# Performance work log

Measured on AMD Instinct MI355X. Metric: run time of the kernel, lower is better.

## Reference

```python
import jax, jax.numpy as jnp
import numpy as np

DIM = 2048
DIM_VISUAL = 1024
HEADS = 16
DIM_HEAD = 64
INNER = HEADS * DIM_HEAD  # 1024
EPS = 1e-5


def setup_inputs() -> dict:
    key = jax.random.key(0)
    ks = jax.random.split(key, 6)
    y = jax.random.normal(ks[0], (4, 2048, DIM), dtype=jnp.float32)
    visual_features = jax.random.normal(ks[1], (4, 8, 64, DIM_VISUAL), dtype=jnp.float32)
    ln_g = jnp.ones((DIM,), dtype=jnp.float32)
    ln_b = jnp.zeros((DIM,), dtype=jnp.float32)
    Wq = jax.random.normal(ks[2], (DIM, INNER), dtype=jnp.float32) * 0.02
    Wkv = jax.random.normal(ks[3], (DIM_VISUAL, 2 * INNER), dtype=jnp.float32) * 0.02
    Wo = jax.random.normal(ks[4], (INNER, DIM), dtype=jnp.float32) * 0.02
    return {"y": y, "visual_features": visual_features, "ln_g": ln_g, "ln_b": ln_b,
            "Wq": Wq, "Wkv": Wkv, "Wo": Wo}


def reference(y, visual_features, ln_g, ln_b, Wq, Wkv, Wo):
    scale = DIM_HEAD ** (-0.5)
    b, t, nq, dv = visual_features.shape
    # LayerNorm over last dim
    mu = jnp.mean(y, axis=-1, keepdims=True)
    var = jnp.mean(jnp.square(y - mu), axis=-1, keepdims=True)
    yn = (y - mu) * jax.lax.rsqrt(var + EPS) * ln_g + ln_b
    q = (yn @ Wq) * scale                      # (b, n, inner)
    vis = visual_features.reshape(b, t * nq, dv)
    kv = vis @ Wkv                             # (b, m, 2*inner)
    k, v = jnp.split(kv, 2, axis=-1)
    # split heads: b n (h d) -> b h n d
    split = lambda x: x.reshape(x.shape[0], x.shape[1], HEADS, DIM_HEAD).transpose(0, 2, 1, 3)
    q, k, v = split(q), split(k), split(v)
    sim = jnp.einsum('bhid,bhjd->bhij', q, k)
    alphas = jax.nn.softmax(sim, axis=-1)      # amax-subtract softmax (stable)
    out = jnp.einsum('bhij,bhjd->bhid', alphas, v)
    out = out.transpose(0, 2, 1, 3).reshape(out.shape[0], out.shape[2], INNER)
    return out @ Wo
```

## Files before the change

kernel.cpp:

```cpp
#include <hip/hip_runtime.h>
#include <stdint.h>

typedef unsigned short u16;
typedef __bf16 bfrag __attribute__((ext_vector_type(8)));
typedef float f32x4 __attribute__((ext_vector_type(4)));
typedef u16 u16x4 __attribute__((ext_vector_type(4)));

__device__ __forceinline__ float bf2f(u16 u) {
  union { unsigned i; float f; } x; x.i = ((unsigned)u) << 16; return x.f;
}
__device__ __forceinline__ u16 f2bf(float f) {
  union { unsigned i; float f; } x; x.f = f;
  unsigned r = x.i + 0x7fffu + ((x.i >> 16) & 1u);
  return (u16)(r >> 16);
}
__device__ __forceinline__ unsigned packbf(float lo, float hi) {
  return (unsigned)f2bf(lo) | ((unsigned)f2bf(hi) << 16);
}

__device__ __forceinline__ f32x4 mfma16(bfrag a, bfrag b, f32x4 c) {
  return __builtin_amdgcn_mfma_f32_16x16x32_bf16(a, b, c, 0, 0, 0);
}

__device__ __forceinline__ void gl_lds16(const u16* g, const u16* l) {
  __builtin_amdgcn_global_load_lds(
      (const __attribute__((address_space(1))) unsigned int*)g,
      (__attribute__((address_space(3))) unsigned int*)l, 16, 0, 0);
}

__device__ __forceinline__ void xcd_swizzle(int& bx, int& by) {
  int gx = gridDim.x, nwg = gx * gridDim.y;
  int flat = by * gx + bx;
  int cpx = nwg >> 3;
  int swz = (flat & 7) * cpx + (flat >> 3);
  bx = swz % gx;
  by = swz / gx;
}

__global__ __launch_bounds__(256) void k_transpose(const float* __restrict__ in,
                                                   u16* __restrict__ out, int R, int C) {
  __shared__ u16 tile[32][33];
  int c0 = blockIdx.x * 32, r0 = blockIdx.y * 32;
  int tx = threadIdx.x, ty = threadIdx.y;
#pragma unroll
  for (int i = 0; i < 4; ++i)
    tile[ty + i * 8][tx] = f2bf(in[(size_t)(r0 + ty + i * 8) * C + c0 + tx]);
  __syncthreads();
#pragma unroll
  for (int i = 0; i < 4; ++i)
    out[(size_t)(c0 + ty + i * 8) * R + r0 + tx] = tile[tx][ty + i * 8];
}

__global__ __launch_bounds__(256) void k_cast(const float* __restrict__ in,
                                              u16* __restrict__ out, int n8) {
  int i = blockIdx.x * 256 + threadIdx.x;
  if (i >= n8) return;
  float4 a = *(const float4*)(in + (size_t)i * 8);
  float4 b = *(const float4*)(in + (size_t)i * 8 + 4);
  uint4 ov; u16* po = (u16*)&ov;
  po[0] = f2bf(a.x); po[1] = f2bf(a.y); po[2] = f2bf(a.z); po[3] = f2bf(a.w);
  po[4] = f2bf(b.x); po[5] = f2bf(b.y); po[6] = f2bf(b.z); po[7] = f2bf(b.w);
  *(uint4*)(out + (size_t)i * 8) = ov;
}

__global__ __launch_bounds__(256) void k_layernorm(const float* __restrict__ y,
                                                   const float* __restrict__ g,
                                                   const float* __restrict__ bb,
                                                   u16* __restrict__ yn) {
  int row = blockIdx.x, t = threadIdx.x;
  const float* yr = y + (size_t)row * 2048 + t * 8;
  float4 v0 = *(const float4*)(yr);
  float4 v1 = *(const float4*)(yr + 4);
  float x[8] = {v0.x, v0.y, v0.z, v0.w, v1.x, v1.y, v1.z, v1.w};
  float s = 0.f, ss = 0.f;
#pragma unroll
  for (int j = 0; j < 8; ++j) { s += x[j]; ss += x[j] * x[j]; }
#pragma unroll
  for (int off = 32; off > 0; off >>= 1) {
    s += __shfl_down(s, off);
    ss += __shfl_down(ss, off);
  }
  __shared__ float rs[4], rq[4];
  int lane = t & 63, wid = t >> 6;
  if (lane == 0) { rs[wid] = s; rq[wid] = ss; }
  __syncthreads();
  float S = rs[0] + rs[1] + rs[2] + rs[3];
  float Q = rq[0] + rq[1] + rq[2] + rq[3];
  float mean = S * (1.f / 2048.f);
  float var = Q * (1.f / 2048.f) - mean * mean;
  float rstd = rsqrtf(var + 1e-5f);
  float4 g0 = *(const float4*)(g + t * 8);
  float4 g1 = *(const float4*)(g + t * 8 + 4);
  float4 b0 = *(const float4*)(bb + t * 8);
  float4 b1 = *(const float4*)(bb + t * 8 + 4);
  float gg[8] = {g0.x, g0.y, g0.z, g0.w, g1.x, g1.y, g1.z, g1.w};
  float bv[8] = {b0.x, b0.y, b0.z, b0.w, b1.x, b1.y, b1.z, b1.w};
  uint4 ov; u16* po = (u16*)&ov;
#pragma unroll
  for (int j = 0; j < 8; ++j)
    po[j] = f2bf((x[j] - mean) * rstd * gg[j] + bv[j]);
  *(uint4*)(yn + (size_t)row * 2048 + t * 8) = ov;
}

template <bool F32OUT>
__global__ __launch_bounds__(256) void k_gemm_bt(const u16* __restrict__ A,
                                                 const u16* __restrict__ Bt,
                                                 void* __restrict__ Cv,
                                                 int M, int N, int K, float scale) {
  __shared__ __align__(16) u16 As[2][128 * 64];
  __shared__ __align__(16) u16 Bs[2][128 * 64];
  int t = threadIdx.x, lane = t & 63, wid = t >> 6;
  int wm = wid >> 1, wn = wid & 1;
  int bx = blockIdx.x, by = blockIdx.y;
  xcd_swizzle(bx, by);
  int m0 = by * 128, n0 = bx * 128;
  int lr = lane & 15, lg = lane >> 4;
  int sk = lr & 7;

  f32x4 acc[4][4];
#pragma unroll
  for (int i = 0; i < 4; ++i)
#pragma unroll
    for (int j = 0; j < 4; ++j) acc[i][j] = (f32x4){0.f, 0.f, 0.f, 0.f};

  int srow[4], scol[4], sbase[4];
#pragma unroll
  for (int j = 0; j < 4; ++j) {
    int s0 = (wid * 4 + j) * 64;
    int s = s0 + lane;
    srow[j] = s >> 3;
    scol[j] = ((s & 7) ^ (srow[j] & 7)) * 8;
    sbase[j] = s0 * 8;
  }

#pragma unroll
  for (int j = 0; j < 4; ++j) {
    gl_lds16(A + (size_t)(m0 + srow[j]) * K + scol[j], As[0] + sbase[j]);
    gl_lds16(Bt + (size_t)(n0 + srow[j]) * K + scol[j], Bs[0] + sbase[j]);
  }
  __syncthreads();

  int nk = K >> 6;
  for (int kt = 0; kt < nk; ++kt) {
    int cur = kt & 1;
    if (kt + 1 < nk) {
      int k0 = (kt + 1) << 6;
#pragma unroll
      for (int j = 0; j < 4; ++j) {
        gl_lds16(A + (size_t)(m0 + srow[j]) * K + k0 + scol[j], As[cur ^ 1] + sbase[j]);
        gl_lds16(Bt + (size_t)(n0 + srow[j]) * K + k0 + scol[j], Bs[cur ^ 1] + sbase[j]);
      }
    }
    const u16* as = As[cur];
    const u16* bs = Bs[cur];
#pragma unroll
    for (int kk = 0; kk < 2; ++kk) {
      bfrag a[4], b[4];
#pragma unroll
      for (int i = 0; i < 4; ++i)
        a[i] = *(const bfrag*)(as + (wm * 64 + i * 16 + lr) * 64 + (((kk * 4 + lg) ^ sk) * 8));
#pragma unroll
      for (int j = 0; j < 4; ++j)
        b[j] = *(const bfrag*)(bs + (wn * 64 + j * 16 + lr) * 64 + (((kk * 4 + lg) ^ sk) * 8));
#pragma unroll
      for (int i = 0; i < 4; ++i)
#pragma unroll
        for (int j = 0; j < 4; ++j)
          acc[i][j] = mfma16(a[i], b[j], acc[i][j]);
    }
    if (kt + 1 < nk) __syncthreads();
  }
#pragma unroll
  for (int i = 0; i < 4; ++i)
#pragma unroll
    for (int j = 0; j < 4; ++j) {
      int r0 = m0 + wm * 64 + i * 16 + lg * 4;
      int c0 = n0 + wn * 64 + j * 16 + lr;
#pragma unroll
      for (int r = 0; r < 4; ++r) {
        float v = scale * acc[i][j][r];
        if (F32OUT)
          ((float*)Cv)[(size_t)(r0 + r) * N + c0] = v;
        else
          ((u16*)Cv)[(size_t)(r0 + r) * N + c0] = f2bf(v);
      }
    }
}

__global__ __launch_bounds__(256) void k_gemm_kv(const u16* __restrict__ A,
                                                 const u16* __restrict__ Bt,
                                                 u16* __restrict__ Kb,
                                                 u16* __restrict__ Vtb) {
  const int K = 1024;
  __shared__ __align__(16) u16 As[2][128 * 64];
  __shared__ __align__(16) u16 Bs[2][128 * 64];
  int t = threadIdx.x, lane = t & 63, wid = t >> 6;
  int wm = wid >> 1, wn = wid & 1;
  int bx = blockIdx.x, by = blockIdx.y;
  xcd_swizzle(bx, by);
  int m0 = by * 128, n0 = bx * 128;
  int lr = lane & 15, lg = lane >> 4;
  int sk = lr & 7;

  f32x4 acc[4][4];
#pragma unroll
  for (int i = 0; i < 4; ++i)
#pragma unroll
    for (int j = 0; j < 4; ++j) acc[i][j] = (f32x4){0.f, 0.f, 0.f, 0.f};

  int srow[4], scol[4], sbase[4];
#pragma unroll
  for (int j = 0; j < 4; ++j) {
    int s0 = (wid * 4 + j) * 64;
    int s = s0 + lane;
    srow[j] = s >> 3;
    scol[j] = ((s & 7) ^ (srow[j] & 7)) * 8;
    sbase[j] = s0 * 8;
  }

#pragma unroll
  for (int j = 0; j < 4; ++j) {
    gl_lds16(A + (size_t)(m0 + srow[j]) * K + scol[j], As[0] + sbase[j]);
    gl_lds16(Bt + (size_t)(n0 + srow[j]) * K + scol[j], Bs[0] + sbase[j]);
  }
  __syncthreads();

  int nk = K >> 6;
  for (int kt = 0; kt < nk; ++kt) {
    int cur = kt & 1;
    if (kt + 1 < nk) {
      int k0 = (kt + 1) << 6;
#pragma unroll
      for (int j = 0; j < 4; ++j) {
        gl_lds16(A + (size_t)(m0 + srow[j]) * K + k0 + scol[j], As[cur ^ 1] + sbase[j]);
        gl_lds16(Bt + (size_t)(n0 + srow[j]) * K + k0 + scol[j], Bs[cur ^ 1] + sbase[j]);
      }
    }
    const u16* as = As[cur];
    const u16* bs = Bs[cur];
#pragma unroll
    for (int kk = 0; kk < 2; ++kk) {
      bfrag a[4], b[4];
#pragma unroll
      for (int i = 0; i < 4; ++i)
        a[i] = *(const bfrag*)(as + (wm * 64 + i * 16 + lr) * 64 + (((kk * 4 + lg) ^ sk) * 8));
#pragma unroll
      for (int j = 0; j < 4; ++j)
        b[j] = *(const bfrag*)(bs + (wn * 64 + j * 16 + lr) * 64 + (((kk * 4 + lg) ^ sk) * 8));
#pragma unroll
      for (int i = 0; i < 4; ++i)
#pragma unroll
        for (int j = 0; j < 4; ++j)
          acc[i][j] = mfma16(a[i], b[j], acc[i][j]);
    }
    if (kt + 1 < nk) __syncthreads();
  }
#pragma unroll
  for (int i = 0; i < 4; ++i)
#pragma unroll
    for (int j = 0; j < 4; ++j) {
      int r0 = m0 + wm * 64 + i * 16 + lg * 4;
      int c0 = n0 + wn * 64 + j * 16 + lr;
      if (c0 < 1024) {
#pragma unroll
        for (int r = 0; r < 4; ++r)
          Kb[(size_t)(r0 + r) * 1024 + c0] = f2bf(acc[i][j][r]);
      } else {
        int d = c0 - 1024;
        int hh = d >> 6, dd = d & 63;
        int bq = r0 >> 9, kvp = r0 & 511;
        u16x4 pk;
#pragma unroll
        for (int r = 0; r < 4; ++r) pk[r] = f2bf(acc[i][j][r]);
        *(u16x4*)(Vtb + ((size_t)(bq * 16 + hh) * 64 + dd) * 512 + kvp) = pk;
      }
    }
}

__global__ __launch_bounds__(256, 2) void k_attn(const u16* __restrict__ q,
                                                 const u16* __restrict__ kb,
                                                 const u16* __restrict__ vt,
                                                 u16* __restrict__ ao) {
  __shared__ __align__(16) u16 Ks[2][128 * 64];
  __shared__ __align__(16) u16 Vt[2][64 * 128];
  int t = threadIdx.x, lane = t & 63, wid = t >> 6;
  int lr = lane & 15, lg = lane >> 4;
  int sk = lr & 7;
  int a_ = lg >> 1, b_ = lg & 1;
  int bh = blockIdx.y, b = bh >> 4, h = bh & 15;
  int q0 = blockIdx.x * 128 + wid * 32;

  const u16* qg = q + (size_t)(b * 2048 + q0) * 1024 + h * 64;
  bfrag qf[2][2];
#pragma unroll
  for (int rt = 0; rt < 2; ++rt)
#pragma unroll
    for (int kk = 0; kk < 2; ++kk)
      qf[rt][kk] = *(const bfrag*)(qg + (size_t)(rt * 16 + lr) * 1024 + kk * 32 + lg * 8);

  f32x4 o[2][4];
#pragma unroll
  for (int rt = 0; rt < 2; ++rt)
#pragma unroll
    for (int dt = 0; dt < 4; ++dt) o[rt][dt] = (f32x4){0.f, 0.f, 0.f, 0.f};
  float m_s[2] = {-1e30f, -1e30f}, l_s[2] = {0.f, 0.f};

  const u16* kgb = kb + (size_t)(b * 512) * 1024 + h * 64;
  const u16* vgb = vt + (size_t)bh * 64 * 512;

  int krow[4], kcol[4], kbase[4];
#pragma unroll
  for (int j = 0; j < 4; ++j) {
    int g = wid * 4 + j;
    int s = g * 64 + lane;
    krow[j] = s >> 3;
    kcol[j] = ((s & 7) ^ (krow[j] & 7)) * 8;
    kbase[j] = g * 512;
  }
  int vd = (threadIdx.x >> 4) & 3;

#pragma unroll
  for (int j = 0; j < 4; ++j)
    gl_lds16(kgb + (size_t)krow[j] * 1024 + kcol[j], Ks[0] + kbase[j]);
#pragma unroll
  for (int j = 0; j < 4; ++j) {
    int g = wid * 4 + j;
    int d = g * 4 + (lane >> 4);
    int p = lane & 15;
    gl_lds16(vgb + (size_t)d * 512 + ((p ^ (d & 7)) * 8), Vt[0] + g * 512);
  }
  __syncthreads();

  for (int it = 0; it < 4; ++it) {
    int cur = it & 1;
    if (it + 1 < 4) {
      int kv1 = (it + 1) * 128;
#pragma unroll
      for (int j = 0; j < 4; ++j)
        gl_lds16(kgb + (size_t)(kv1 + krow[j]) * 1024 + kcol[j], Ks[cur ^ 1] + kbase[j]);
#pragma unroll
      for (int j = 0; j < 4; ++j) {
        int g = wid * 4 + j;
        int d = g * 4 + (lane >> 4);
        int p = lane & 15;
        gl_lds16(vgb + (size_t)d * 512 + kv1 + ((p ^ (d & 7)) * 8), Vt[cur ^ 1] + g * 512);
      }
    }
    const u16* ks = Ks[cur];
    const u16* vtl = Vt[cur];

#pragma unroll
    for (int rt = 0; rt < 2; ++rt) {
      f32x4 s[8];
#pragma unroll
      for (int ct = 0; ct < 8; ++ct) {
        s[ct] = (f32x4){0.f, 0.f, 0.f, 0.f};
#pragma unroll
        for (int kk = 0; kk < 2; ++kk) {
          bfrag kf = *(const bfrag*)(ks + (ct * 16 + lr) * 64 + (((kk * 4 + lg) ^ sk) * 8));
          s[ct] = mfma16(kf, qf[rt][kk], s[ct]);
        }
      }
      float mloc = -1e30f;
#pragma unroll
      for (int ct = 0; ct < 8; ++ct)
#pragma unroll
        for (int r = 0; r < 4; ++r) mloc = fmaxf(mloc, s[ct][r]);
      mloc = fmaxf(mloc, __shfl_xor(mloc, 16));
      mloc = fmaxf(mloc, __shfl_xor(mloc, 32));
      float mn = fmaxf(m_s[rt], mloc);
      float scq = __expf(m_s[rt] - mn);
      float ps = 0.f;
#pragma unroll
      for (int ct = 0; ct < 8; ++ct)
#pragma unroll
        for (int r = 0; r < 4; ++r) {
          float p = __expf(s[ct][r] - mn);
          s[ct][r] = p;
          ps += p;
        }
      ps += __shfl_xor(ps, 16);
      ps += __shfl_xor(ps, 32);
      l_s[rt] = l_s[rt] * scq + ps;
      m_s[rt] = mn;
      float sc4[4];
#pragma unroll
      for (int r = 0; r < 4; ++r) sc4[r] = __shfl(scq, (lane & 48) | (lg * 4 + r));
#pragma unroll
      for (int dt = 0; dt < 4; ++dt)
#pragma unroll
        for (int r = 0; r < 4; ++r) o[rt][dt][r] *= sc4[r];

      unsigned w0[8], w1[8];
#pragma unroll
      for (int ct = 0; ct < 8; ++ct) {
        w0[ct] = packbf(s[ct][0], s[ct][1]);
        w1[ct] = packbf(s[ct][2], s[ct][3]);
      }
      bfrag pf[4];
#pragma unroll
      for (int kt = 0; kt < 4; ++kt) {
        unsigned c0w0 = w0[2 * kt], c0w1 = w1[2 * kt];
        unsigned c1w0 = w0[2 * kt + 1], c1w1 = w1[2 * kt + 1];
        unsigned s0 = a_ ? c0w0 : c1w0;
        unsigned s1 = a_ ? c0w1 : c1w1;
        unsigned k0 = a_ ? c1w0 : c0w0;
        unsigned k1 = a_ ? c1w1 : c0w1;
        unsigned r0 = (unsigned)__shfl_xor((int)s0, 32);
        unsigned r1 = (unsigned)__shfl_xor((int)s1, 32);
        unsigned x0 = (a_ == b_) ? r0 : k0;
        unsigned x1 = (a_ == b_) ? r1 : k1;
        unsigned kk0 = (a_ == b_) ? k0 : r0;
        unsigned kk1 = (a_ == b_) ? k1 : r1;
        unsigned q0_ = (unsigned)__shfl_xor((int)x0, 16);
        unsigned q1_ = (unsigned)__shfl_xor((int)x1, 16);
        union { unsigned u[4]; bfrag f; } uf;
        uf.u[0] = b_ ? q0_ : kk0;
        uf.u[1] = b_ ? q1_ : kk1;
        uf.u[2] = b_ ? kk0 : q0_;
        uf.u[3] = b_ ? kk1 : q1_;
        pf[kt] = uf.f;
      }
#pragma unroll
      for (int dt = 0; dt < 4; ++dt)
#pragma unroll
        for (int kt = 0; kt < 4; ++kt) {
          int d = dt * 16 + lr;
          bfrag vfb = *(const bfrag*)(vtl + d * 128 + (((kt * 4 + lg) ^ (d & 7)) * 8));
          o[rt][dt] = mfma16(pf[kt], vfb, o[rt][dt]);
        }
    }
    if (it + 1 < 4) __syncthreads();
  }

#pragma unroll
  for (int rt = 0; rt < 2; ++rt) {
    float invq = 1.f / l_s[rt];
    float i4[4];
#pragma unroll
    for (int r = 0; r < 4; ++r) i4[r] = __shfl(invq, (lane & 48) | (lg * 4 + r));
#pragma unroll
    for (int dt = 0; dt < 4; ++dt)
#pragma unroll
      for (int r = 0; r < 4; ++r)
        ao[(size_t)(b * 2048 + q0 + rt * 16 + lg * 4 + r) * 1024 + h * 64 + dt * 16 + lr] =
            f2bf(o[rt][dt][r] * i4[r]);
  }
}

extern "C" void kernel_launch(void* const* d_in, const int* in_sizes, int n_in,
                              void* d_out, int out_size, void* d_ws, size_t ws_size,
                              hipStream_t stream) {
  const float* y   = (const float*)d_in[0];
  const float* vf  = (const float*)d_in[1];
  const float* g   = (const float*)d_in[2];
  const float* bb  = (const float*)d_in[3];
  const float* Wq  = (const float*)d_in[4];
  const float* Wkv = (const float*)d_in[5];
  const float* Wo  = (const float*)d_in[6];
  float* out = (float*)d_out;
  char* ws = (char*)d_ws;

  u16* qb   = (u16*)(ws + 0ull);
  u16* kbuf = (u16*)(ws + 16777216ull);
  u16* vtb  = (u16*)(ws + 20971520ull);
  u16* aob  = (u16*)(ws + 25165824ull);
  u16* wqT  = (u16*)(ws + 41943040ull);
  u16* wkvT = (u16*)(ws + 46137344ull);
  u16* woT  = (u16*)(ws + 50331648ull);
  u16* vfb  = (u16*)(ws + 54525952ull);
  u16* yn = (u16*)d_out;

  dim3 tb(32, 8, 1);
  k_transpose<<<dim3(1024 / 32, 2048 / 32, 1), tb, 0, stream>>>(Wq, wqT, 2048, 1024);
  k_transpose<<<dim3(2048 / 32, 1024 / 32, 1), tb, 0, stream>>>(Wkv, wkvT, 1024, 2048);
  k_transpose<<<dim3(2048 / 32, 1024 / 32, 1), tb, 0, stream>>>(Wo, woT, 1024, 2048);
  k_cast<<<(2048 * 1024 / 8 + 255) / 256, 256, 0, stream>>>(vf, vfb, 2048 * 1024 / 8);
  k_layernorm<<<8192, 256, 0, stream>>>(y, g, bb, yn);
  k_gemm_bt<false><<<dim3(1024 / 128, 8192 / 128, 1), 256, 0, stream>>>(yn, wqT, qb, 8192, 1024, 2048, 0.125f);
  k_gemm_kv<<<dim3(2048 / 128, 2048 / 128, 1), 256, 0, stream>>>(vfb, wkvT, kbuf, vtb);
  k_attn<<<dim3(16, 64, 1), 256, 0, stream>>>(qb, kbuf, vtb, aob);
  k_gemm_bt<true><<<dim3(2048 / 128, 8192 / 128, 1), 256, 0, stream>>>(aob, woT, out, 8192, 2048, 1024, 1.0f);
}
```

Measured before the change: 178.1 us.

## Deepen GEMM prefetch pipeline and share K/V fragments across query tiles

```diff
diff --git a/kernel.cpp b/kernel.cpp
--- a/kernel.cpp
+++ b/kernel.cpp
@@ -102,74 +102,91 @@
   *(uint4*)(yn + (size_t)row * 2048 + t * 8) = ov;
 }
 
+__device__ __forceinline__ void gemm_pipe(const u16* __restrict__ A,
+                                          const u16* __restrict__ Bt,
+                                          int K, int m0, int n0,
+                                          int wm, int wn, int lr, int lg,
+                                          int wid, int lane,
+                                          f32x4 (&acc)[4][4]) {
+  __shared__ __align__(16) u16 As[2][128 * 64];
+  __shared__ __align__(16) u16 Bs[2][128 * 64];
+  int sk = lr & 7;
+  int srow[4], scol[4], sbase[4];
+#pragma unroll
+  for (int j = 0; j < 4; ++j) {
+    int s0 = (wid * 4 + j) * 64;
+    int s = s0 + lane;
+    srow[j] = s >> 3;
+    scol[j] = ((s & 7) ^ (srow[j] & 7)) * 8;
+    sbase[j] = s0 * 8;
+  }
+  int nk = K >> 6;
+#pragma unroll
+  for (int pt = 0; pt < 2; ++pt)
+#pragma unroll
+    for (int j = 0; j < 4; ++j) {
+      gl_lds16(A + (size_t)(m0 + srow[j]) * K + pt * 64 + scol[j], As[pt] + sbase[j]);
+      gl_lds16(Bt + (size_t)(n0 + srow[j]) * K + pt * 64 + scol[j], Bs[pt] + sbase[j]);
+    }
+  for (int tt = 0; tt < nk; ++tt) {
+    if (tt + 1 < nk)
+      asm volatile("s_waitcnt vmcnt(8)" ::: "memory");
+    else
+      asm volatile("s_waitcnt vmcnt(0)" ::: "memory");
+    __builtin_amdgcn_s_barrier();
+    __builtin_amdgcn_sched_barrier(0);
+    const u16* as = As[tt & 1];
+    const u16* bs = Bs[tt & 1];
+#pragma unroll
+    for (int kk = 0; kk < 2; ++kk) {
+      bfrag a[4], b[4];
+#pragma unroll
+      for (int i = 0; i < 4; ++i)
+        a[i] = *(const bfrag*)(as + (wm * 64 + i * 16 + lr) * 64 + (((kk * 4 + lg) ^ sk) * 8));
+#pragma unroll
+      for (int j = 0; j < 4; ++j)
+        b[j] = *(const bfrag*)(bs + (wn * 64 + j * 16 + lr) * 64 + (((kk * 4 + lg) ^ sk) * 8));
+      __builtin_amdgcn_s_setprio(1);
+#pragma unroll
+      for (int i = 0; i < 4; ++i)
+#pragma unroll
+        for (int j = 0; j < 4; ++j)
+          acc[i][j] = mfma16(a[i], b[j], acc[i][j]);
+      __builtin_amdgcn_s_setprio(0);
+    }
+    asm volatile("s_waitcnt lgkmcnt(0)" ::: "memory");
+    __builtin_amdgcn_s_barrier();
+    __builtin_amdgcn_sched_barrier(0);
+    if (tt + 2 < nk) {
+      int k0 = (tt + 2) * 64;
+#pragma unroll
+      for (int j = 0; j < 4; ++j) {
+        gl_lds16(A + (size_t)(m0 + srow[j]) * K + k0 + scol[j], As[tt & 1] + sbase[j]);
+        gl_lds16(Bt + (size_t)(n0 + srow[j]) * K + k0 + scol[j], Bs[tt & 1] + sbase[j]);
+      }
+    }
+  }
+}
+
 template <bool F32OUT>
 __global__ __launch_bounds__(256) void k_gemm_bt(const u16* __restrict__ A,
                                                  const u16* __restrict__ Bt,
                                                  void* __restrict__ Cv,
                                                  int M, int N, int K, float scale) {
-  __shared__ __align__(16) u16 As[2][128 * 64];
-  __shared__ __align__(16) u16 Bs[2][128 * 64];
   int t = threadIdx.x, lane = t & 63, wid = t >> 6;
   int wm = wid >> 1, wn = wid & 1;
   int bx = blockIdx.x, by = blockIdx.y;
   xcd_swizzle(bx, by);
   int m0 = by * 128, n0 = bx * 128;
   int lr = lane & 15, lg = lane >> 4;
-  int sk = lr & 7;
-
   f32x4 acc[4][4];
 #pragma unroll
   for (int i = 0; i < 4; ++i)
 #pragma unroll
     for (int j = 0; j < 4; ++j) acc[i][j] = (f32x4){0.f, 0.f, 0.f, 0.f};
 
-  int srow[4], scol[4], sbase[4];
-#pragma unroll
-  for (int j = 0; j < 4; ++j) {
-    int s0 = (wid * 4 + j) * 64;
-    int s = s0 + lane;
-    srow[j] = s >> 3;
-    scol[j] = ((s & 7) ^ (srow[j] & 7)) * 8;
-    sbase[j] = s0 * 8;
-  }
-
-#pragma unroll
-  for (int j = 0; j < 4; ++j) {
-    gl_lds16(A + (size_t)(m0 + srow[j]) * K + scol[j], As[0] + sbase[j]);
-    gl_lds16(Bt + (size_t)(n0 + srow[j]) * K + scol[j], Bs[0] + sbase[j]);
-  }
-  __syncthreads();
-
-  int nk = K >> 6;
-  for (int kt = 0; kt < nk; ++kt) {
-    int cur = kt & 1;
-    if (kt + 1 < nk) {
-      int k0 = (kt + 1) << 6;
-#pragma unroll
-      for (int j = 0; j < 4; ++j) {
-        gl_lds16(A + (size_t)(m0 + srow[j]) * K + k0 + scol[j], As[cur ^ 1] + sbase[j]);
-        gl_lds16(Bt + (size_t)(n0 + srow[j]) * K + k0 + scol[j], Bs[cur ^ 1] + sbase[j]);
-      }
-    }
-    const u16* as = As[cur];
-    const u16* bs = Bs[cur];
-#pragma unroll
-    for (int kk = 0; kk < 2; ++kk) {
-      bfrag a[4], b[4];
-#pragma unroll
-      for (int i = 0; i < 4; ++i)
-        a[i] = *(const bfrag*)(as + (wm * 64 + i * 16 + lr) * 64 + (((kk * 4 + lg) ^ sk) * 8));
-#pragma unroll
-      for (int j = 0; j < 4; ++j)
-        b[j] = *(const bfrag*)(bs + (wn * 64 + j * 16 + lr) * 64 + (((kk * 4 + lg) ^ sk) * 8));
-#pragma unroll
-      for (int i = 0; i < 4; ++i)
-#pragma unroll
-        for (int j = 0; j < 4; ++j)
-          acc[i][j] = mfma16(a[i], b[j], acc[i][j]);
-    }
-    if (kt + 1 < nk) __syncthreads();
-  }
+  gemm_pipe(A, Bt, K, m0, n0, wm, wn, lr, lg, wid, lane, acc);
+
 #pragma unroll
   for (int i = 0; i < 4; ++i)
 #pragma unroll
@@ -192,69 +209,20 @@
                                                  u16* __restrict__ Kb,
                                                  u16* __restrict__ Vtb) {
   const int K = 1024;
-  __shared__ __align__(16) u16 As[2][128 * 64];
-  __shared__ __align__(16) u16 Bs[2][128 * 64];
   int t = threadIdx.x, lane = t & 63, wid = t >> 6;
   int wm = wid >> 1, wn = wid & 1;
   int bx = blockIdx.x, by = blockIdx.y;
   xcd_swizzle(bx, by);
   int m0 = by * 128, n0 = bx * 128;
   int lr = lane & 15, lg = lane >> 4;
-  int sk = lr & 7;
-
   f32x4 acc[4][4];
 #pragma unroll
   for (int i = 0; i < 4; ++i)
 #pragma unroll
     for (int j = 0; j < 4; ++j) acc[i][j] = (f32x4){0.f, 0.f, 0.f, 0.f};
 
-  int srow[4], scol[4], sbase[4];
-#pragma unroll
-  for (int j = 0; j < 4; ++j) {
-    int s0 = (wid * 4 + j) * 64;
-    int s = s0 + lane;
-    srow[j] = s >> 3;
-    scol[j] = ((s & 7) ^ (srow[j] & 7)) * 8;
-    sbase[j] = s0 * 8;
-  }
-
-#pragma unroll
-  for (int j = 0; j < 4; ++j) {
-    gl_lds16(A + (size_t)(m0 + srow[j]) * K + scol[j], As[0] + sbase[j]);
-    gl_lds16(Bt + (size_t)(n0 + srow[j]) * K + scol[j], Bs[0] + sbase[j]);
-  }
-  __syncthreads();
-
-  int nk = K >> 6;
-  for (int kt = 0; kt < nk; ++kt) {
-    int cur = kt & 1;
-    if (kt + 1 < nk) {
-      int k0 = (kt + 1) << 6;
-#pragma unroll
-      for (int j = 0; j < 4; ++j) {
-        gl_lds16(A + (size_t)(m0 + srow[j]) * K + k0 + scol[j], As[cur ^ 1] + sbase[j]);
-        gl_lds16(Bt + (size_t)(n0 + srow[j]) * K + k0 + scol[j], Bs[cur ^ 1] + sbase[j]);
-      }
-    }
-    const u16* as = As[cur];
-    const u16* bs = Bs[cur];
-#pragma unroll
-    for (int kk = 0; kk < 2; ++kk) {
-      bfrag a[4], b[4];
-#pragma unroll
-      for (int i = 0; i < 4; ++i)
-        a[i] = *(const bfrag*)(as + (wm * 64 + i * 16 + lr) * 64 + (((kk * 4 + lg) ^ sk) * 8));
-#pragma unroll
-      for (int j = 0; j < 4; ++j)
-        b[j] = *(const bfrag*)(bs + (wn * 64 + j * 16 + lr) * 64 + (((kk * 4 + lg) ^ sk) * 8));
-#pragma unroll
-      for (int i = 0; i < 4; ++i)
-#pragma unroll
-        for (int j = 0; j < 4; ++j)
-          acc[i][j] = mfma16(a[i], b[j], acc[i][j]);
-    }
-    if (kt + 1 < nk) __syncthreads();
-  }
+  gemm_pipe(A, Bt, K, m0, n0, wm, wn, lr, lg, wid, lane, acc);
+
 #pragma unroll
   for (int i = 0; i < 4; ++i)
 #pragma unroll
@@ -317,7 +285,6 @@
     kcol[j] = ((s & 7) ^ (krow[j] & 7)) * 8;
     kbase[j] = g * 512;
   }
-  int vd = (threadIdx.x >> 4) & 3;
 
 #pragma unroll
   for (int j = 0; j < 4; ++j)
@@ -349,23 +316,30 @@
     const u16* ks = Ks[cur];
     const u16* vtl = Vt[cur];
 
+    f32x4 s[2][8];
+#pragma unroll
+    for (int rt = 0; rt < 2; ++rt)
+#pragma unroll
+      for (int ct = 0; ct < 8; ++ct) s[rt][ct] = (f32x4){0.f, 0.f, 0.f, 0.f};
+    __builtin_amdgcn_s_setprio(1);
+#pragma unroll
+    for (int ct = 0; ct < 8; ++ct)
+#pragma unroll
+      for (int kk = 0; kk < 2; ++kk) {
+        bfrag kf = *(const bfrag*)(ks + (ct * 16 + lr) * 64 + (((kk * 4 + lg) ^ sk) * 8));
+        s[0][ct] = mfma16(kf, qf[0][kk], s[0][ct]);
+        s[1][ct] = mfma16(kf, qf[1][kk], s[1][ct]);
+      }
+    __builtin_amdgcn_s_setprio(0);
+
+    bfrag pf[2][4];
 #pragma unroll
     for (int rt = 0; rt < 2; ++rt) {
-      f32x4 s[8];
-#pragma unroll
-      for (int ct = 0; ct < 8; ++ct) {
-        s[ct] = (f32x4){0.f, 0.f, 0.f, 0.f};
-#pragma unroll
-        for (int kk = 0; kk < 2; ++kk) {
-          bfrag kf = *(const bfrag*)(ks + (ct * 16 + lr) * 64 + (((kk * 4 + lg) ^ sk) * 8));
-          s[ct] = mfma16(kf, qf[rt][kk], s[ct]);
-        }
-      }
       float mloc = -1e30f;
 #pragma unroll
       for (int ct = 0; ct < 8; ++ct)
 #pragma unroll
-        for (int r = 0; r < 4; ++r) mloc = fmaxf(mloc, s[ct][r]);
+        for (int r = 0; r < 4; ++r) mloc = fmaxf(mloc, s[rt][ct][r]);
       mloc = fmaxf(mloc, __shfl_xor(mloc, 16));
       mloc = fmaxf(mloc, __shfl_xor(mloc, 32));
       float mn = fmaxf(m_s[rt], mloc);
@@ -375,8 +349,8 @@
       for (int ct = 0; ct < 8; ++ct)
 #pragma unroll
         for (int r = 0; r < 4; ++r) {
-          float p = __expf(s[ct][r] - mn);
-          s[ct][r] = p;
+          float p = __expf(s[rt][ct][r] - mn);
+          s[rt][ct][r] = p;
           ps += p;
         }
       ps += __shfl_xor(ps, 16);
@@ -394,10 +368,9 @@
       unsigned w0[8], w1[8];
 #pragma unroll
       for (int ct = 0; ct < 8; ++ct) {
-        w0[ct] = packbf(s[ct][0], s[ct][1]);
-        w1[ct] = packbf(s[ct][2], s[ct][3]);
-      }
-      bfrag pf[4];
+        w0[ct] = packbf(s[rt][ct][0], s[rt][ct][1]);
+        w1[ct] = packbf(s[rt][ct][2], s[rt][ct][3]);
+      }
 #pragma unroll
       for (int kt = 0; kt < 4; ++kt) {
         unsigned c0w0 = w0[2 * kt], c0w1 = w1[2 * kt];
@@ -419,17 +392,22 @@
         uf.u[1] = b_ ? q1_ : kk1;
         uf.u[2] = b_ ? kk0 : q0_;
         uf.u[3] = b_ ? kk1 : q1_;
-        pf[kt] = uf.f;
-      }
-#pragma unroll
-      for (int dt = 0; dt < 4; ++dt)
-#pragma unroll
-        for (int kt = 0; kt < 4; ++kt) {
-          int d = dt * 16 + lr;
-          bfrag vfb = *(const bfrag*)(vtl + d * 128 + (((kt * 4 + lg) ^ (d & 7)) * 8));
-          o[rt][dt] = mfma16(pf[kt], vfb, o[rt][dt]);
-        }
-    }
+        pf[rt][kt] = uf.f;
+      }
+    }
+
+    __builtin_amdgcn_s_setprio(1);
+#pragma unroll
+    for (int dt = 0; dt < 4; ++dt)
+#pragma unroll
+      for (int kt = 0; kt < 4; ++kt) {
+        int d = dt * 16 + lr;
+        bfrag vfb = *(const bfrag*)(vtl + d * 128 + (((kt * 4 + lg) ^ (d & 7)) * 8));
+        o[0][dt] = mfma16(pf[0][kt], vfb, o[0][dt]);
+        o[1][dt] = mfma16(pf[1][kt], vfb, o[1][dt]);
+      }
+    __builtin_amdgcn_s_setprio(0);
+
     if (it + 1 < 4) __syncthreads();
   }
 
```

New measurement: 174.6 us. 2.0% less time.
